# Kernel optimization log

Measured on AMD Instinct MI355X. Metric: run time of the kernel, lower is better.

The kernel has to match this reference:

```python
import jax, jax.numpy as jnp
import numpy as np

N_LAYER, N_HEAD, D_MODEL, D_FF = 6, 16, 1024, 4096
D_HEAD = D_MODEL // N_HEAD            # 64
M_FEAT = 2 * D_MODEL // N_HEAD        # 128, favor_feature_dims default
CHUNK = 128                           # chunk size for causal linear attention
LN_EPS = 1e-5
ATT_EPS = 1e-6                        # fast-transformers CausalLinearAttention eps
B, S = 4, 2048


def _layer_norm(x, g, b):
    mu = x.mean(-1, keepdims=True)
    var = ((x - mu) ** 2).mean(-1, keepdims=True)
    return (x - mu) * jax.lax.rsqrt(var + LN_EPS) * g + b


def _favor_phi(x, omega):
    # x: [B,H,S,Dh]; omega: [Dh, M//2]. FAVOR positive (hyperbolic) random
    # features: phi(x) = [exp(u - |x|^2/2), exp(-u - |x|^2/2)] / sqrt(M),
    # with x pre-scaled by sqrt(softmax_temp), softmax_temp = 1/sqrt(Dh).
    x = x * (D_HEAD ** -0.25)
    u = jnp.einsum('bhsd,dm->bhsm', x, omega)
    nrm = 0.5 * jnp.sum(x * x, axis=-1, keepdims=True)
    phi = jnp.concatenate([jnp.exp(u - nrm), jnp.exp(-u - nrm)], axis=-1)
    return phi * (M_FEAT ** -0.5)


def _causal_linear_attention(Qp, Kp, V):
    # Qp,Kp: [B,H,S,M] nonnegative features; V: [B,H,S,Dh].
    # out_i = phi(q_i)^T S_i / (phi(q_i)^T Z_i + eps),
    # S_i = sum_{j<=i} phi(k_j) v_j^T, Z_i = sum_{j<=i} phi(k_j).
    # Chunked: exclusive chunk prefix sums + masked intra-chunk matmul.
    b, h, s, m = Qp.shape
    d = V.shape[-1]
    c = s // CHUNK
    Qc = Qp.reshape(b, h, c, CHUNK, m)
    Kc = Kp.reshape(b, h, c, CHUNK, m)
    Vc = V.reshape(b, h, c, CHUNK, d)
    kv = jnp.einsum('bhclm,bhcld->bhcmd', Kc, Vc)   # per-chunk K^T V
    ksum = Kc.sum(axis=3)                            # [b,h,c,m]
    kv_pre = jnp.cumsum(kv, axis=2) - kv             # exclusive prefix over chunks
    ks_pre = jnp.cumsum(ksum, axis=2) - ksum
    scores = jnp.einsum('bhcim,bhcjm->bhcij', Qc, Kc)
    mask = jnp.tril(jnp.ones((CHUNK, CHUNK), bool))
    scores = jnp.where(mask, scores, 0.0)            # causal within chunk
    num = (jnp.einsum('bhcij,bhcjd->bhcid', scores, Vc)
           + jnp.einsum('bhcim,bhcmd->bhcid', Qc, kv_pre))
    den = scores.sum(-1) + jnp.einsum('bhcim,bhcm->bhci', Qc, ks_pre)
    out = num / (den[..., None] + ATT_EPS)
    return out.reshape(b, h, s, d)


def _forward(x, Wq, bq, Wk, bk, Wv, bv, Wo, bo, omega,
             g1, be1, W1, bf1, W2, bf2, g2, be2):
    bsz, slen, _ = x.shape
    out = x
    for l in range(N_LAYER):
        def proj(W, bvec):
            y = jnp.einsum('bsd,de->bse', out, W) + bvec
            return y.reshape(bsz, slen, N_HEAD, D_HEAD).transpose(0, 2, 1, 3)
        q = proj(Wq[l], bq[l])
        k = proj(Wk[l], bk[l])
        v = proj(Wv[l], bv[l])
        Qp = _favor_phi(q, omega[l])
        Kp = _favor_phi(k, omega[l])
        a = _causal_linear_attention(Qp, Kp, v)
        a = a.transpose(0, 2, 1, 3).reshape(bsz, slen, D_MODEL)
        a = jnp.einsum('bsd,de->bse', a, Wo[l]) + bo[l]
        h1 = _layer_norm(out + a, g1[l], be1[l])          # post-norm residual 1
        y = jax.nn.relu(jnp.einsum('bsd,df->bsf', h1, W1[l]) + bf1[l])
        y = jnp.einsum('bsf,fd->bsd', y, W2[l]) + bf2[l]
        out = _layer_norm(h1 + y, g2[l], be2[l])          # post-norm residual 2
    return out


def setup_inputs() -> dict:
    key = jax.random.key(0)
    ks = jax.random.split(key, 12)
    s = D_MODEL ** -0.5
    f32 = jnp.float32
    return {
        "x": jax.random.normal(ks[0], (B, S, D_MODEL), f32),
        "Wq": jax.random.normal(ks[1], (N_LAYER, D_MODEL, D_MODEL), f32) * s,
        "bq": jnp.zeros((N_LAYER, D_MODEL), f32),
        "Wk": jax.random.normal(ks[2], (N_LAYER, D_MODEL, D_MODEL), f32) * s,
        "bk": jnp.zeros((N_LAYER, D_MODEL), f32),
        "Wv": jax.random.normal(ks[3], (N_LAYER, D_MODEL, D_MODEL), f32) * s,
        "bv": jnp.zeros((N_LAYER, D_MODEL), f32),
        "Wo": jax.random.normal(ks[4], (N_LAYER, D_MODEL, D_MODEL), f32) * s,
        "bo": jnp.zeros((N_LAYER, D_MODEL), f32),
        "omega": jax.random.normal(ks[5], (N_LAYER, D_HEAD, M_FEAT // 2), f32),
        "g1": jnp.ones((N_LAYER, D_MODEL), f32),
        "be1": jnp.zeros((N_LAYER, D_MODEL), f32),
        "W1": jax.random.normal(ks[6], (N_LAYER, D_MODEL, D_FF), f32) * s,
        "bf1": jnp.zeros((N_LAYER, D_FF), f32),
        "W2": jax.random.normal(ks[7], (N_LAYER, D_FF, D_MODEL), f32) * (D_FF ** -0.5),
        "bf2": jnp.zeros((N_LAYER, D_MODEL), f32),
        "g2": jnp.ones((N_LAYER, D_MODEL), f32),
        "be2": jnp.zeros((N_LAYER, D_MODEL), f32),
    }


def reference(x, Wq, bq, Wk, bk, Wv, bv, Wo, bo, omega,
              g1, be1, W1, bf1, W2, bf2, g2, be2):
    return _forward(x, Wq, bq, Wk, bk, Wv, bv, Wo, bo, omega,
                    g1, be1, W1, bf1, W2, bf2, g2, be2)
```

## Files before the change

### kernel.cpp

```cpp
#include <hip/hip_runtime.h>

typedef unsigned short u16;
typedef __attribute__((ext_vector_type(8))) short bf16x8;
typedef __attribute__((ext_vector_type(4))) float f32x4;

#define DEV __device__ __forceinline__

DEV float b2f(u16 h){ return __uint_as_float(((unsigned)h) << 16); }
DEV u16 f2b(float f){ unsigned u = __float_as_uint(f); u += 0x7FFFu + ((u >> 16) & 1u); return (u16)(u >> 16); }

DEV void gload16(const u16* g, u16* l){
  __builtin_amdgcn_global_load_lds((const __attribute__((address_space(1))) unsigned*)g,
                                   (__attribute__((address_space(3))) unsigned*)l, 16, 0, 0);
}

__global__ __launch_bounds__(256) void wtrans(const float* __restrict__ src, u16* __restrict__ dst,
                                              int K, int N, float scale){
  __shared__ float tile[32][33];
  int k0 = blockIdx.x * 32, n0 = blockIdx.y * 32;
  int tid = threadIdx.x;
#pragma unroll
  for (int i = 0; i < 4; i++){
    int idx = tid + i * 256;
    int r = idx >> 5, c = idx & 31;
    tile[r][c] = src[(size_t)(k0 + r) * N + n0 + c];
  }
  __syncthreads();
#pragma unroll
  for (int i = 0; i < 4; i++){
    int idx = tid + i * 256;
    int r = idx >> 5, c = idx & 31;
    dst[(size_t)(n0 + r) * K + k0 + c] = f2b(tile[c][r] * scale);
  }
}

__global__ __launch_bounds__(256) void cvt16(const float* __restrict__ src, u16* __restrict__ dst){
  size_t i = ((size_t)blockIdx.x * 256 + threadIdx.x) * 4;
  float4 f = *(const float4*)(src + i);
  ushort4 o = make_ushort4(f2b(f.x), f2b(f.y), f2b(f.z), f2b(f.w));
  *(ushort4*)(dst + i) = o;
}

__global__ void catbias(const float* __restrict__ bq, const float* __restrict__ bk,
                        const float* __restrict__ bv, float* __restrict__ bcat){
  int i = blockIdx.x * 256 + threadIdx.x;
  if (i >= 6 * 3072) return;
  int l = i / 3072, j = i % 3072;
  float v = (j < 1024) ? bq[l * 1024 + j] : (j < 2048) ? bk[l * 1024 + j - 1024] : bv[l * 1024 + j - 2048];
  bcat[i] = v;
}

__global__ void fillv(float* __restrict__ p, float v, int n){
  int i = blockIdx.x * 256 + threadIdx.x;
  if (i < n) p[i] = v;
}

DEV int swz(int r){ return (r & 3) ^ ((r >> 2) & 3); }

template<int EPI>
__global__ __launch_bounds__(256) void gemm_bt(const u16* __restrict__ A, const u16* __restrict__ Bt,
                                               const float* __restrict__ bias, void* __restrict__ outp,
                                               int M, int N, int K, int ldA, int ldB){
  __shared__ __align__(16) u16 As[2][4096];
  __shared__ __align__(16) u16 Bs[2][4096];
  const int tid = threadIdx.x;
  const int lane = tid & 63;
  const int w = tid >> 6;
  const int wm = w >> 1, wn = w & 1;
  int nx = gridDim.x;
  int nwg = nx * gridDim.y;
  int lin = blockIdx.y * nx + blockIdx.x;
  int cpx = nwg >> 3;
  int sw = (lin & 7) * cpx + (lin >> 3);
  const int m0 = (sw / nx) * 128;
  const int n0 = (sw % nx) * 128;

  int r0 = tid >> 2, c0 = tid & 3;
  int r1 = r0 + 64;
  int cs0 = c0 ^ swz(r0);
  int cs1 = c0 ^ swz(r1);
  const u16* ag0 = A + (size_t)(m0 + r0) * ldA + cs0 * 8;
  const u16* ag1 = A + (size_t)(m0 + r1) * ldA + cs1 * 8;
  const u16* bg0 = Bt + (size_t)(n0 + r0) * ldB + cs0 * 8;
  const u16* bg1 = Bt + (size_t)(n0 + r1) * ldB + cs1 * 8;

  f32x4 acc[4][4] = {};
  const int KT = K >> 5;

  gload16(ag0, &As[0][w * 512]);
  gload16(ag1, &As[0][2048 + w * 512]);
  gload16(bg0, &Bs[0][w * 512]);
  gload16(bg1, &Bs[0][2048 + w * 512]);

  for (int kt = 0; kt < KT; kt++){
    int cur = kt & 1;
    if (kt + 1 < KT){
      int ko = (kt + 1) << 5;
      gload16(ag0 + ko, &As[cur ^ 1][w * 512]);
      gload16(ag1 + ko, &As[cur ^ 1][2048 + w * 512]);
      gload16(bg0 + ko, &Bs[cur ^ 1][w * 512]);
      gload16(bg1 + ko, &Bs[cur ^ 1][2048 + w * 512]);
      asm volatile("s_waitcnt vmcnt(4)" ::: "memory");
    } else {
      asm volatile("s_waitcnt vmcnt(0)" ::: "memory");
    }
    __builtin_amdgcn_s_barrier();
    bf16x8 fa[4], fb[4];
#pragma unroll
    for (int m = 0; m < 4; m++){
      int row = wm * 64 + m * 16 + (lane & 15);
      int cc = (lane >> 4) ^ swz(row);
      fa[m] = *(const bf16x8*)(&As[cur][row * 32 + cc * 8]);
    }
#pragma unroll
    for (int n = 0; n < 4; n++){
      int row = wn * 64 + n * 16 + (lane & 15);
      int cc = (lane >> 4) ^ swz(row);
      fb[n] = *(const bf16x8*)(&Bs[cur][row * 32 + cc * 8]);
    }
#pragma unroll
    for (int m = 0; m < 4; m++)
#pragma unroll
      for (int n = 0; n < 4; n++)
        acc[m][n] = __builtin_amdgcn_mfma_f32_16x16x32_bf16(fa[m], fb[n], acc[m][n], 0, 0, 0);
    asm volatile("s_waitcnt lgkmcnt(0)" ::: "memory");
    __builtin_amdgcn_s_barrier();
  }

#pragma unroll
  for (int m = 0; m < 4; m++){
    int rowb = m0 + wm * 64 + m * 16 + ((lane >> 4) << 2);
#pragma unroll
    for (int n = 0; n < 4; n++){
      int col = n0 + wn * 64 + n * 16 + (lane & 15);
      float bv = bias[col];
      if (EPI == 5 && col >= 2048){
        int cv = col - 2048, hh = cv >> 6, dh = cv & 63;
        int bIdx = rowb >> 11, s4 = rowb & 2047;
        ushort4 pk = make_ushort4(f2b(acc[m][n][0] + bv), f2b(acc[m][n][1] + bv),
                                  f2b(acc[m][n][2] + bv), f2b(acc[m][n][3] + bv));
        *(ushort4*)&((u16*)outp + 16777216)[((size_t)(bIdx * 16 + hh) * 64 + dh) * 2048 + s4] = pk;
      } else {
#pragma unroll
        for (int r = 0; r < 4; r++){
          float v = acc[m][n][r] + bv;
          int rr = rowb + r;
          if (EPI == 5){
            u16* dst0 = (u16*)outp + (col < 1024 ? 0 : 8388608);
            int cv = col & 1023, hh = cv >> 6, dh = cv & 63;
            int bIdx = rr >> 11, s = rr & 2047;
            dst0[(((size_t)(bIdx * 16 + hh) * 2048 + s) << 6) + dh] = f2b(v);
          } else if (EPI == 1){
            ((float*)outp)[(size_t)rr * N + col] = v;
          } else {
            ((u16*)outp)[(size_t)rr * N + col] = f2b(v > 0.f ? v : 0.f);
          }
        }
      }
    }
  }
}

__global__ __launch_bounds__(256) void phi2(const u16* __restrict__ qb, const u16* __restrict__ kb,
                                            const u16* __restrict__ omT,
                                            u16* __restrict__ Qp, u16* __restrict__ Kp){
  __shared__ __align__(16) u16 qs[128 * 64];
  __shared__ __align__(16) u16 wl[64 * 64];
  __shared__ __align__(16) u16 ph[128 * 128];
  __shared__ float part[2][128];
  __shared__ float nrm[128];
  int tid = threadIdx.x, w = tid >> 6, lane = tid & 63;
  int blk = blockIdx.x;
  const u16* src; u16* dst; int row0;
  if (blk < 1024){ src = qb; dst = Qp; row0 = blk * 128; }
  else           { src = kb; dst = Kp; row0 = (blk - 1024) * 128; }
  const u16* g = src + (size_t)row0 * 64;
#pragma unroll
  for (int i = 0; i < 4; i++){
    int id = tid * 4 + i;
    int r = id >> 3, kc = id & 7;
    *(bf16x8*)(qs + r * 64 + ((kc ^ (r & 7)) << 3)) = *(const bf16x8*)(g + r * 64 + kc * 8);
  }
#pragma unroll
  for (int i = 0; i < 2; i++){
    int id = tid * 2 + i;
    int m = id >> 3, kc = id & 7;
    *(bf16x8*)(wl + m * 64 + ((kc ^ (m & 7)) << 3)) = *(const bf16x8*)(omT + id * 8);
  }
  __syncthreads();
  {
    int r = tid & 127, half = tid >> 7;
    float s = 0.f;
#pragma unroll
    for (int j = 0; j < 4; j++){
      int kc = half * 4 + j;
      bf16x8 v = *(const bf16x8*)(qs + r * 64 + ((kc ^ (r & 7)) << 3));
#pragma unroll
      for (int e = 0; e < 8; e++){ float f = b2f((u16)v[e]); s += f * f; }
    }
    part[half][r] = s;
  }
  __syncthreads();
  if (tid < 128) nrm[tid] = 0.0625f * (part[0][tid] + part[1][tid]);
  __syncthreads();
  f32x4 acc[2][4] = {};
#pragma unroll
  for (int kt = 0; kt < 2; kt++){
    int kc = kt * 4 + (lane >> 4);
    bf16x8 fa[2], fb[4];
#pragma unroll
    for (int mt = 0; mt < 2; mt++){
      int r = w * 32 + mt * 16 + (lane & 15);
      fa[mt] = *(const bf16x8*)(qs + r * 64 + ((kc ^ (r & 7)) << 3));
    }
#pragma unroll
    for (int nt = 0; nt < 4; nt++){
      int m = nt * 16 + (lane & 15);
      fb[nt] = *(const bf16x8*)(wl + m * 64 + ((kc ^ (m & 7)) << 3));
    }
#pragma unroll
    for (int mt = 0; mt < 2; mt++)
#pragma unroll
      for (int nt = 0; nt < 4; nt++)
        acc[mt][nt] = __builtin_amdgcn_mfma_f32_16x16x32_bf16(fa[mt], fb[nt], acc[mt][nt], 0, 0, 0);
  }
  const float LNC = -2.4260151319598086f;
#pragma unroll
  for (int mt = 0; mt < 2; mt++)
#pragma unroll
    for (int nt = 0; nt < 4; nt++)
#pragma unroll
      for (int r4 = 0; r4 < 4; r4++){
        int r = w * 32 + mt * 16 + ((lane >> 4) << 2) + r4;
        int m = nt * 16 + (lane & 15);
        float u = acc[mt][nt][r4];
        float nr = nrm[r];
        ph[r * 128 + m]      = f2b(__expf(u - nr + LNC));
        ph[r * 128 + 64 + m] = f2b(__expf(-u - nr + LNC));
      }
  __syncthreads();
  u16* go = dst + (size_t)row0 * 128;
#pragma unroll
  for (int i = 0; i < 8; i++){
    int id = i * 256 + tid;
    *(bf16x8*)(go + id * 8) = *(const bf16x8*)(ph + id * 8);
  }
}

__global__ __launch_bounds__(256) void kvchunk(const u16* __restrict__ Kp, const u16* __restrict__ vt,
                                               float* __restrict__ kv, float* __restrict__ ksum){
  __shared__ __align__(16) u16 Ks[128 * 128];
  __shared__ __align__(16) u16 Vst[64 * 128];
  int blk = blockIdx.x; int bh = blk >> 4, c = blk & 15;
  int tid = threadIdx.x;
  size_t base = (size_t)bh * 2048 + c * 128;
  const u16* Kc = Kp + base * 128;
  const u16* vtc = vt + (size_t)bh * 64 * 2048 + c * 128;
  {
    int j = tid >> 1, half = tid & 1;
#pragma unroll
    for (int i = 0; i < 8; i++)
      *(bf16x8*)(Ks + j * 128 + half * 64 + i * 8) = *(const bf16x8*)(Kc + j * 128 + half * 64 + i * 8);
#pragma unroll
    for (int i = 0; i < 4; i++){
      int id = tid * 4 + i;
      int d = id >> 4, mc = id & 15;
      *(bf16x8*)(Vst + d * 128 + mc * 8) = *(const bf16x8*)(vtc + (size_t)d * 2048 + mc * 8);
    }
  }
  __syncthreads();
  int tm = tid & 15, td = tid >> 4;
  int mbase = tm * 8, dbase = td * 4;
  float acc[8][4] = {};
  float ks[8] = {};
  for (int i = 0; i < 128; i++){
    bf16x8 kk = *(const bf16x8*)(Ks + i * 128 + mbase);
    float kf[8];
#pragma unroll
    for (int e = 0; e < 8; e++) kf[e] = b2f((u16)kk[e]);
    float vf[4];
#pragma unroll
    for (int e = 0; e < 4; e++) vf[e] = b2f(Vst[(dbase + e) * 128 + i]);
#pragma unroll
    for (int a = 0; a < 8; a++){
      ks[a] += kf[a];
#pragma unroll
      for (int bb = 0; bb < 4; bb++) acc[a][bb] += kf[a] * vf[bb];
    }
  }
  float* kvout = kv + ((size_t)bh * 16 + c) * 8192;
#pragma unroll
  for (int a = 0; a < 8; a++)
#pragma unroll
    for (int bb = 0; bb < 4; bb++)
      kvout[(size_t)(dbase + bb) * 128 + mbase + a] = acc[a][bb];
  if (td == 0){
    float* kso = ksum + ((size_t)bh * 16 + c) * 128;
#pragma unroll
    for (int a = 0; a < 8; a++) kso[mbase + a] = ks[a];
  }
}

__global__ __launch_bounds__(256) void kvscan(float* __restrict__ kv, float* __restrict__ ksum){
  int bh = blockIdx.x;
  int p = blockIdx.y;
  int tid = threadIdx.x;
  if (p < 8){
    size_t base = (size_t)bh * 16 * 8192;
    int idx0 = p * 1024 + tid;
    for (int rep = 0; rep < 4; rep++){
      int idx = idx0 + rep * 256;
      float run = 0.f;
#pragma unroll
      for (int c = 0; c < 16; c++){
        size_t off = base + (size_t)c * 8192 + idx;
        float v = kv[off]; kv[off] = run; run += v;
      }
    }
  } else if (tid < 128){
    size_t base = (size_t)bh * 16 * 128;
    float run = 0.f;
#pragma unroll
    for (int c = 0; c < 16; c++){
      size_t off = base + c * 128 + tid;
      float v = ksum[off]; ksum[off] = run; run += v;
    }
  }
}

__global__ __launch_bounds__(512) void attn_fused(const u16* __restrict__ Qp, const u16* __restrict__ Kp,
                                                  const u16* __restrict__ vt, const float* __restrict__ kvp,
                                                  const float* __restrict__ ksum, u16* __restrict__ aout){
  __shared__ __align__(16) u16 sm[53248];
  int blk = blockIdx.x, bh = blk >> 4, c = blk & 15;
  int b = bh >> 4, h = bh & 15;
  int tid = threadIdx.x, w = tid >> 6, lane = tid & 63;
  size_t base = (size_t)bh * 2048 + c * 128;
  const u16* Qc = Qp + base * 128;
  const u16* Kc = Kp + base * 128;
  const u16* vtc = vt + (size_t)bh * 64 * 2048 + c * 128;
  const float* kvc = kvp + ((size_t)bh * 16 + c) * 8192;
  const float* ksc = ksum + ((size_t)bh * 16 + c) * 128;
  u16* Qs = sm;
  u16* Ks = sm + 16384;
  u16* B2 = sm + 32768;

#pragma unroll
  for (int i = 0; i < 4; i++){
    int id = tid * 4 + i;
    int r = id >> 4, kc = id & 15;
    int swo = (kc ^ (r & 15)) << 3;
    *(bf16x8*)(Qs + r * 128 + swo) = *(const bf16x8*)(Qc + (size_t)r * 128 + kc * 8);
    *(bf16x8*)(Ks + r * 128 + swo) = *(const bf16x8*)(Kc + (size_t)r * 128 + kc * 8);
  }
#pragma unroll
  for (int i = 0; i < 2; i++){
    int id = tid * 2 + i;
    int d = id >> 4, kc = id & 15;
    *(bf16x8*)(B2 + d * 256 + ((kc ^ (d & 31)) << 3)) = *(const bf16x8*)(vtc + (size_t)d * 2048 + kc * 8);
  }
#pragma unroll
  for (int i = 0; i < 2; i++){
    int id = tid * 2 + i;
    int d = id >> 4, mc = id & 15;
    const float* s8 = kvc + d * 128 + mc * 8;
    float4 f0 = *(const float4*)(s8);
    float4 f1 = *(const float4*)(s8 + 4);
    bf16x8 pk;
    pk[0] = (short)f2b(f0.x); pk[1] = (short)f2b(f0.y); pk[2] = (short)f2b(f0.z); pk[3] = (short)f2b(f0.w);
    pk[4] = (short)f2b(f1.x); pk[5] = (short)f2b(f1.y); pk[6] = (short)f2b(f1.z); pk[7] = (short)f2b(f1.w);
    int kc = 16 + mc;
    *(bf16x8*)(B2 + d * 256 + ((kc ^ (d & 31)) << 3)) = pk;
  }
  {
    int row = 64 + (tid >> 5), kc = tid & 31;
    bf16x8 pk = {};
    if (row == 64){
      if (kc < 16){
#pragma unroll
        for (int e = 0; e < 8; e++) pk[e] = (short)0x3F80;
      } else {
        const float* s8 = ksc + (kc - 16) * 8;
        float4 f0 = *(const float4*)(s8);
        float4 f1 = *(const float4*)(s8 + 4);
        pk[0] = (short)f2b(f0.x); pk[1] = (short)f2b(f0.y); pk[2] = (short)f2b(f0.z); pk[3] = (short)f2b(f0.w);
        pk[4] = (short)f2b(f1.x); pk[5] = (short)f2b(f1.y); pk[6] = (short)f2b(f1.z); pk[7] = (short)f2b(f1.w);
      }
    }
    *(bf16x8*)(B2 + row * 256 + ((kc ^ (row & 31)) << 3)) = pk;
  }
  __syncthreads();

  int wm = w >> 2, wn = w & 3;
  f32x4 acc1[4][2] = {};
#pragma unroll
  for (int kk = 0; kk < 4; kk++){
    int kc = kk * 4 + (lane >> 4);
    bf16x8 fa[4], fb[2];
#pragma unroll
    for (int m = 0; m < 4; m++){
      int row = wm * 64 + m * 16 + (lane & 15);
      fa[m] = *(const bf16x8*)(Qs + row * 128 + ((kc ^ (row & 15)) << 3));
    }
#pragma unroll
    for (int n = 0; n < 2; n++){
      int row = wn * 32 + n * 16 + (lane & 15);
      fb[n] = *(const bf16x8*)(Ks + row * 128 + ((kc ^ (row & 15)) << 3));
    }
#pragma unroll
    for (int m = 0; m < 4; m++)
#pragma unroll
      for (int n = 0; n < 2; n++)
        acc1[m][n] = __builtin_amdgcn_mfma_f32_16x16x32_bf16(fa[m], fb[n], acc1[m][n], 0, 0, 0);
  }
  __syncthreads();

#pragma unroll
  for (int m = 0; m < 4; m++)
#pragma unroll
    for (int n = 0; n < 2; n++)
#pragma unroll
      for (int r = 0; r < 4; r++){
        int i = wm * 64 + m * 16 + ((lane >> 4) << 2) + r;
        int j = wn * 32 + n * 16 + (lane & 15);
        float v = (j <= i) ? acc1[m][n][r] : 0.f;
        Ks[i * 128 + (((j >> 3) ^ (i & 15)) << 3) + (j & 7)] = f2b(v);
      }
  __syncthreads();

  f32x4 acc2[5] = {};
#pragma unroll
  for (int kk = 0; kk < 8; kk++){
    int kc = kk * 4 + (lane >> 4);
    int rowA = w * 16 + (lane & 15);
    bf16x8 fa2;
    if (kk < 4) fa2 = *(const bf16x8*)(Ks + rowA * 128 + ((kc ^ (rowA & 15)) << 3));
    else        fa2 = *(const bf16x8*)(Qs + rowA * 128 + (((kc - 16) ^ (rowA & 15)) << 3));
#pragma unroll
    for (int n = 0; n < 5; n++){
      int d = n * 16 + (lane & 15);
      bf16x8 fb2 = *(const bf16x8*)(B2 + d * 256 + ((kc ^ (d & 31)) << 3));
      acc2[n] = __builtin_amdgcn_mfma_f32_16x16x32_bf16(fa2, fb2, acc2[n], 0, 0, 0);
    }
  }

  float dd[4];
#pragma unroll
  for (int r = 0; r < 4; r++) dd[r] = __shfl(acc2[4][r], lane & 48) + 1e-6f;
  size_t obase = ((size_t)b * 2048 + c * 128) * 1024 + (size_t)h * 64;
#pragma unroll
  for (int n = 0; n < 4; n++)
#pragma unroll
    for (int r = 0; r < 4; r++){
      int i = w * 16 + ((lane >> 4) << 2) + r;
      int d = n * 16 + (lane & 15);
      aout[obase + (size_t)i * 1024 + d] = f2b(acc2[n][r] / dd[r]);
    }
}

__global__ __launch_bounds__(256) void ln_kernel(const float* __restrict__ X1, const float* __restrict__ X2,
                                                 const float* __restrict__ g, const float* __restrict__ bb,
                                                 float* __restrict__ outf, u16* __restrict__ outb){
  __shared__ float red[2][4];
  int row = blockIdx.x, tid = threadIdx.x, w = tid >> 6, lane = tid & 63;
  size_t ro = (size_t)row * 1024 + tid * 4;
  float4 a = *(const float4*)(X1 + ro);
  float4 b4 = *(const float4*)(X2 + ro);
  float x0 = a.x + b4.x, x1 = a.y + b4.y, x2 = a.z + b4.z, x3 = a.w + b4.w;
  float s1 = x0 + x1 + x2 + x3;
  float s2 = x0 * x0 + x1 * x1 + x2 * x2 + x3 * x3;
#pragma unroll
  for (int off = 32; off; off >>= 1){ s1 += __shfl_xor(s1, off); s2 += __shfl_xor(s2, off); }
  if (lane == 0){ red[0][w] = s1; red[1][w] = s2; }
  __syncthreads();
  float t1 = red[0][0] + red[0][1] + red[0][2] + red[0][3];
  float t2 = red[1][0] + red[1][1] + red[1][2] + red[1][3];
  float mu = t1 * (1.f / 1024.f);
  float var = t2 * (1.f / 1024.f) - mu * mu;
  float rs = rsqrtf(var + 1e-5f);
  float4 gv = *(const float4*)(g + tid * 4);
  float4 bv = *(const float4*)(bb + tid * 4);
  float o0 = (x0 - mu) * rs * gv.x + bv.x;
  float o1 = (x1 - mu) * rs * gv.y + bv.y;
  float o2 = (x2 - mu) * rs * gv.z + bv.z;
  float o3 = (x3 - mu) * rs * gv.w + bv.w;
  *(float4*)(outf + ro) = make_float4(o0, o1, o2, o3);
  *(ushort4*)(outb + ro) = make_ushort4(f2b(o0), f2b(o1), f2b(o2), f2b(o3));
}

extern "C" void kernel_launch(void* const* d_in, const int* in_sizes, int n_in,
                              void* d_out, int out_size, void* d_ws, size_t ws_size,
                              hipStream_t stream){
  (void)in_sizes; (void)n_in;
  const float* x   = (const float*)d_in[0];
  const float* Wq  = (const float*)d_in[1];
  const float* bq  = (const float*)d_in[2];
  const float* Wk  = (const float*)d_in[3];
  const float* bk  = (const float*)d_in[4];
  const float* Wv  = (const float*)d_in[5];
  const float* bv  = (const float*)d_in[6];
  const float* Wo  = (const float*)d_in[7];
  const float* bo  = (const float*)d_in[8];
  const float* om  = (const float*)d_in[9];
  const float* g1  = (const float*)d_in[10];
  const float* be1 = (const float*)d_in[11];
  const float* W1  = (const float*)d_in[12];
  const float* bf1 = (const float*)d_in[13];
  const float* W2  = (const float*)d_in[14];
  const float* bf2 = (const float*)d_in[15];
  const float* g2  = (const float*)d_in[16];
  const float* be2 = (const float*)d_in[17];

  char* ws = (char*)d_ws;
  size_t off = 0;
  auto alloc = [&](size_t bytes) -> void* {
    void* p = ws + off; off += (bytes + 255) & ~(size_t)255; return p;
  };
  u16* Wcat = (u16*)alloc(3072ull * 1024 * 2);
  u16* Wot  = (u16*)alloc(1024ull * 1024 * 2);
  u16* W1t  = (u16*)alloc(4096ull * 1024 * 2);
  u16* W2t  = (u16*)alloc(1024ull * 4096 * 2);
  u16* omT  = (u16*)alloc(64ull * 64 * 2);
  float* bcat = (float*)alloc(6ull * 3072 * 4);
  u16* Xb  = (u16*)alloc(8192ull * 1024 * 2);
  u16* qb  = (u16*)alloc(131072ull * 64 * 2);
  u16* kb  = (u16*)alloc(131072ull * 64 * 2);
  u16* vt  = (u16*)alloc(131072ull * 64 * 2);
  u16* Qp  = (u16*)alloc(131072ull * 128 * 2);
  u16* Kp  = (u16*)alloc(131072ull * 128 * 2);
  float* ksum = (float*)alloc(64ull * 16 * 128 * 4);

  if (off > ws_size){
    fillv<<<(out_size + 255) / 256, 256, 0, stream>>>((float*)d_out, (float)(ws_size >> 20), out_size);
    return;
  }

  float* kvbuf = (float*)qb;
  float* woout = (float*)qb;
  u16*  ybuf  = qb;
  float* h1    = (float*)Kp;
  float* w2out = (float*)d_out;
  float* resid = (float*)d_out;

  cvt16<<<8192, 256, 0, stream>>>(x, Xb);
  catbias<<<72, 256, 0, stream>>>(bq, bk, bv, bcat);

  const float* Xsrc = x;
  for (int l = 0; l < 6; l++){
    size_t o1k = (size_t)l * 1024 * 1024;
    size_t o4k = (size_t)l * 4096 * 1024;
    wtrans<<<dim3(32, 32), 256, 0, stream>>>(Wq + o1k, Wcat, 1024, 1024, 1.f);
    wtrans<<<dim3(32, 32), 256, 0, stream>>>(Wk + o1k, Wcat + 1024ull * 1024, 1024, 1024, 1.f);
    wtrans<<<dim3(32, 32), 256, 0, stream>>>(Wv + o1k, Wcat + 2048ull * 1024, 1024, 1024, 1.f);
    wtrans<<<dim3(32, 32), 256, 0, stream>>>(Wo + o1k, Wot, 1024, 1024, 1.f);
    wtrans<<<dim3(32, 128), 256, 0, stream>>>(W1 + o4k, W1t, 1024, 4096, 1.f);
    wtrans<<<dim3(128, 32), 256, 0, stream>>>(W2 + o4k, W2t, 4096, 1024, 1.f);
    wtrans<<<dim3(2, 2), 256, 0, stream>>>(om + (size_t)l * 4096, omT, 64, 64, 0.35355339059327373f);

    gemm_bt<5><<<dim3(24, 64), 256, 0, stream>>>(Xb, Wcat, bcat + l * 3072, qb, 8192, 3072, 1024, 1024, 1024);
    phi2<<<2048, 256, 0, stream>>>(qb, kb, omT, Qp, Kp);
    kvchunk<<<1024, 256, 0, stream>>>(Kp, vt, kvbuf, ksum);
    kvscan<<<dim3(64, 9), 256, 0, stream>>>(kvbuf, ksum);
    attn_fused<<<1024, 512, 0, stream>>>(Qp, Kp, vt, kvbuf, ksum, Xb);
    gemm_bt<1><<<dim3(8, 64), 256, 0, stream>>>(Xb, Wot, bo + l * 1024, woout, 8192, 1024, 1024, 1024, 1024);
    ln_kernel<<<8192, 256, 0, stream>>>(Xsrc, woout, g1 + l * 1024, be1 + l * 1024, h1, Xb);
    gemm_bt<2><<<dim3(32, 64), 256, 0, stream>>>(Xb, W1t, bf1 + l * 4096, ybuf, 8192, 4096, 1024, 1024, 1024);
    gemm_bt<1><<<dim3(8, 64), 256, 0, stream>>>(ybuf, W2t, bf2 + l * 1024, w2out, 8192, 1024, 4096, 4096, 4096);
    ln_kernel<<<8192, 256, 0, stream>>>(h1, w2out, g2 + l * 1024, be2 + l * 1024, resid, Xb);
    Xsrc = resid;
  }
}
```

Baseline: 2.667 ms.

## Add 256x256 triple-buffered GEMM and store projection outputs in bf16

Adds a 512-thread GEMM kernel with 256x256 tiles, a three-stage global-to-LDS pipeline, XOR-swizzled LDS, tile-order swizzling and raised MFMA priority. It is used for the QKV and FFN-up projections to get more data reuse per tile. The output and FFN-down GEMMs now write bf16 instead of fp32, and layer norm reads them as bf16, which halves that traffic but rounds the residual branch to bf16 before the add. Buffers are reassigned so these bf16 outputs live in Qp.

```diff
diff --git a/kernel.cpp b/kernel.cpp
--- a/kernel.cpp
+++ b/kernel.cpp
@@ -134,6 +134,103 @@
     for (int n = 0; n < 4; n++){
       int col = n0 + wn * 64 + n * 16 + (lane & 15);
       float bv = bias[col];
+#pragma unroll
+      for (int r = 0; r < 4; r++){
+        float v = acc[m][n][r] + bv;
+        int rr = rowb + r;
+        if (EPI == 2) ((u16*)outp)[(size_t)rr * N + col] = f2b(v > 0.f ? v : 0.f);
+        else          ((u16*)outp)[(size_t)rr * N + col] = f2b(v);
+      }
+    }
+  }
+}
+
+template<int EPI>
+__global__ __launch_bounds__(512, 1) void gemm256(const u16* __restrict__ A, const u16* __restrict__ Bt,
+                                                  const float* __restrict__ bias, void* __restrict__ outp,
+                                                  int M, int N, int K, int ldA, int ldB){
+  __shared__ __align__(16) u16 As[3][8192];
+  __shared__ __align__(16) u16 Bs[3][8192];
+  const int tid = threadIdx.x;
+  const int lane = tid & 63;
+  const int w = tid >> 6;
+  const int wm = w >> 2, wn = w & 3;
+  int nx = gridDim.x;
+  int nwg = nx * gridDim.y;
+  int lin = blockIdx.y * nx + blockIdx.x;
+  int cpx = nwg >> 3;
+  int sw = (lin & 7) * cpx + (lin >> 3);
+  const int m0 = (sw / nx) * 256;
+  const int n0 = (sw % nx) * 256;
+
+  int rA0 = tid >> 2, c0 = tid & 3;
+  int rA1 = rA0 + 128;
+  int csA0 = c0 ^ ((rA0 >> 1) & 3);
+  int csA1 = c0 ^ ((rA1 >> 1) & 3);
+  const u16* ag0 = A + (size_t)(m0 + rA0) * ldA + csA0 * 8;
+  const u16* ag1 = A + (size_t)(m0 + rA1) * ldA + csA1 * 8;
+  const u16* bg0 = Bt + (size_t)(n0 + rA0) * ldB + csA0 * 8;
+  const u16* bg1 = Bt + (size_t)(n0 + rA1) * ldB + csA1 * 8;
+
+  f32x4 acc[8][4] = {};
+  const int KT = K >> 5;
+
+#pragma unroll
+  for (int t = 0; t < 2; t++){
+    int ko = t << 5;
+    gload16(ag0 + ko, &As[t][w * 512]);
+    gload16(ag1 + ko, &As[t][4096 + w * 512]);
+    gload16(bg0 + ko, &Bs[t][w * 512]);
+    gload16(bg1 + ko, &Bs[t][4096 + w * 512]);
+  }
+
+  for (int t = 0; t < KT; t++){
+    int buf = t % 3;
+    if (t + 2 < KT){
+      int nb = (t + 2) % 3;
+      int ko = (t + 2) << 5;
+      gload16(ag0 + ko, &As[nb][w * 512]);
+      gload16(ag1 + ko, &As[nb][4096 + w * 512]);
+      gload16(bg0 + ko, &Bs[nb][w * 512]);
+      gload16(bg1 + ko, &Bs[nb][4096 + w * 512]);
+      asm volatile("s_waitcnt vmcnt(8)" ::: "memory");
+    } else if (t + 1 < KT){
+      asm volatile("s_waitcnt vmcnt(4)" ::: "memory");
+    } else {
+      asm volatile("s_waitcnt vmcnt(0)" ::: "memory");
+    }
+    __builtin_amdgcn_s_barrier();
+    bf16x8 fa[8], fb[4];
+#pragma unroll
+    for (int m = 0; m < 8; m++){
+      int row = wm * 128 + m * 16 + (lane & 15);
+      int cc = (lane >> 4) ^ ((row >> 1) & 3);
+      fa[m] = *(const bf16x8*)(&As[buf][row * 32 + cc * 8]);
+    }
+#pragma unroll
+    for (int n = 0; n < 4; n++){
+      int row = wn * 64 + n * 16 + (lane & 15);
+      int cc = (lane >> 4) ^ ((row >> 1) & 3);
+      fb[n] = *(const bf16x8*)(&Bs[buf][row * 32 + cc * 8]);
+    }
+    __builtin_amdgcn_s_setprio(1);
+#pragma unroll
+    for (int m = 0; m < 8; m++)
+#pragma unroll
+      for (int n = 0; n < 4; n++)
+        acc[m][n] = __builtin_amdgcn_mfma_f32_16x16x32_bf16(fa[m], fb[n], acc[m][n], 0, 0, 0);
+    __builtin_amdgcn_s_setprio(0);
+    asm volatile("s_waitcnt lgkmcnt(0)" ::: "memory");
+    __builtin_amdgcn_s_barrier();
+  }
+
+#pragma unroll
+  for (int m = 0; m < 8; m++){
+    int rowb = m0 + wm * 128 + m * 16 + ((lane >> 4) << 2);
+#pragma unroll
+    for (int n = 0; n < 4; n++){
+      int col = n0 + wn * 64 + n * 16 + (lane & 15);
+      float bv = bias[col];
       if (EPI == 5 && col >= 2048){
         int cv = col - 2048, hh = cv >> 6, dh = cv & 63;
         int bIdx = rowb >> 11, s4 = rowb & 2047;
@@ -150,8 +247,6 @@
             int cv = col & 1023, hh = cv >> 6, dh = cv & 63;
             int bIdx = rr >> 11, s = rr & 2047;
             dst0[(((size_t)(bIdx * 16 + hh) * 2048 + s) << 6) + dh] = f2b(v);
-          } else if (EPI == 1){
-            ((float*)outp)[(size_t)rr * N + col] = v;
           } else {
             ((u16*)outp)[(size_t)rr * N + col] = f2b(v > 0.f ? v : 0.f);
           }
@@ -458,15 +553,15 @@
     }
 }
 
-__global__ __launch_bounds__(256) void ln_kernel(const float* __restrict__ X1, const float* __restrict__ X2,
+__global__ __launch_bounds__(256) void ln_kernel(const float* __restrict__ X1, const u16* __restrict__ X2b,
                                                  const float* __restrict__ g, const float* __restrict__ bb,
                                                  float* __restrict__ outf, u16* __restrict__ outb){
   __shared__ float red[2][4];
   int row = blockIdx.x, tid = threadIdx.x, w = tid >> 6, lane = tid & 63;
   size_t ro = (size_t)row * 1024 + tid * 4;
   float4 a = *(const float4*)(X1 + ro);
-  float4 b4 = *(const float4*)(X2 + ro);
-  float x0 = a.x + b4.x, x1 = a.y + b4.y, x2 = a.z + b4.z, x3 = a.w + b4.w;
+  ushort4 bp = *(const ushort4*)(X2b + ro);
+  float x0 = a.x + b2f(bp.x), x1 = a.y + b2f(bp.y), x2 = a.z + b2f(bp.z), x3 = a.w + b2f(bp.w);
   float s1 = x0 + x1 + x2 + x3;
   float s2 = x0 * x0 + x1 * x1 + x2 * x2 + x3 * x3;
 #pragma unroll
@@ -535,12 +630,12 @@
     return;
   }
 
-  float* kvbuf = (float*)qb;
-  float* woout = (float*)qb;
-  u16*  ybuf  = qb;
-  float* h1    = (float*)Kp;
-  float* w2out = (float*)d_out;
-  float* resid = (float*)d_out;
+  float* kvbuf  = (float*)qb;
+  u16*  ybuf   = qb;
+  u16*  wooutb = Qp;
+  u16*  w2outb = Qp + 8388608;
+  float* h1     = (float*)Kp;
+  float* resid  = (float*)d_out;
 
   cvt16<<<8192, 256, 0, stream>>>(x, Xb);
   catbias<<<72, 256, 0, stream>>>(bq, bk, bv, bcat);
@@ -557,16 +652,16 @@
     wtrans<<<dim3(128, 32), 256, 0, stream>>>(W2 + o4k, W2t, 4096, 1024, 1.f);
     wtrans<<<dim3(2, 2), 256, 0, stream>>>(om + (size_t)l * 4096, omT, 64, 64, 0.35355339059327373f);
 
-    gemm_bt<5><<<dim3(24, 64), 256, 0, stream>>>(Xb, Wcat, bcat + l * 3072, qb, 8192, 3072, 1024, 1024, 1024);
+    gemm256<5><<<dim3(12, 32), 512, 0, stream>>>(Xb, Wcat, bcat + l * 3072, qb, 8192, 3072, 1024, 1024, 1024);
     phi2<<<2048, 256, 0, stream>>>(qb, kb, omT, Qp, Kp);
     kvchunk<<<1024, 256, 0, stream>>>(Kp, vt, kvbuf, ksum);
     kvscan<<<dim3(64, 9), 256, 0, stream>>>(kvbuf, ksum);
     attn_fused<<<1024, 512, 0, stream>>>(Qp, Kp, vt, kvbuf, ksum, Xb);
-    gemm_bt<1><<<dim3(8, 64), 256, 0, stream>>>(Xb, Wot, bo + l * 1024, woout, 8192, 1024, 1024, 1024, 1024);
-    ln_kernel<<<8192, 256, 0, stream>>>(Xsrc, woout, g1 + l * 1024, be1 + l * 1024, h1, Xb);
-    gemm_bt<2><<<dim3(32, 64), 256, 0, stream>>>(Xb, W1t, bf1 + l * 4096, ybuf, 8192, 4096, 1024, 1024, 1024);
-    gemm_bt<1><<<dim3(8, 64), 256, 0, stream>>>(ybuf, W2t, bf2 + l * 1024, w2out, 8192, 1024, 4096, 4096, 4096);
-    ln_kernel<<<8192, 256, 0, stream>>>(h1, w2out, g2 + l * 1024, be2 + l * 1024, resid, Xb);
+    gemm_bt<6><<<dim3(8, 64), 256, 0, stream>>>(Xb, Wot, bo + l * 1024, wooutb, 8192, 1024, 1024, 1024, 1024);
+    ln_kernel<<<8192, 256, 0, stream>>>(Xsrc, wooutb, g1 + l * 1024, be1 + l * 1024, h1, Xb);
+    gemm256<2><<<dim3(16, 32), 512, 0, stream>>>(Xb, W1t, bf1 + l * 4096, ybuf, 8192, 4096, 1024, 1024, 1024);
+    gemm_bt<6><<<dim3(8, 64), 256, 0, stream>>>(ybuf, W2t, bf2 + l * 1024, w2outb, 8192, 1024, 4096, 4096, 4096);
+    ln_kernel<<<8192, 256, 0, stream>>>(h1, w2outb, g2 + l * 1024, be2 + l * 1024, resid, Xb);
     Xsrc = resid;
   }
 }
```

New measurement: 2.756 ms. 3.4% more time.
